# Performance work log

Measured on AMD Instinct MI355X. Metric: run time of the kernel, lower is better.

## Reference

```python
import jax, jax.numpy as jnp
import numpy as np

N = 10000   # nodes
E = 160000  # edges (avg degree 16)
C = 128     # channels (multiplicity)
RB = 8      # radial basis size
HID = 64    # radial MLP hidden
AVG_NEIGH = 16.0

# e3nn-style constants: w3j(1,1,0)=delta/sqrt(3); component-normalization path alphas
C_000 = float(np.sqrt(0.5))                 # 0e x 0e -> 0e (two paths into 0e)
C_110 = float(np.sqrt(0.5) / np.sqrt(3.0))  # 1o x 1o -> 0e
C_011 = float(np.sqrt(1.5) / np.sqrt(3.0))  # 0e x 1o -> 1o (sqrt(dim=3 / 2 paths) * w3j)
C_101 = float(np.sqrt(1.5) / np.sqrt(3.0))  # 1o x 0e -> 1o


def setup_inputs() -> dict:
    key = jax.random.key(0)
    ks = jax.random.split(key, 14)
    rn = lambda k, s: jax.random.normal(k, s, dtype=jnp.float32)
    return {
        "node_attrs": rn(ks[0], (N, 10)),            # unused in forward (kept for fidelity)
        "node_feats": rn(ks[1], (N, 4 * C)),          # 128x0e (128) + 128x1o (384)
        "edge_attrs": rn(ks[2], (E, 4)),              # 1x0e + 1x1o spherical harmonics
        "edge_feats": rn(ks[3], (E, RB)),             # radial basis
        "edge_index": jax.random.randint(ks[4], (2, E), 0, N, dtype=jnp.int32),
        # linear_up (per-irrep channel mixing)
        "W_up_s": rn(ks[5], (C, C)),
        "W_up_v": rn(ks[6], (C, C)),
        # radial MLP [RB,64,64,64,weight_numel=4*C]
        "W_mlp1": rn(ks[7], (RB, HID)),
        "W_mlp2": rn(ks[8], (HID, HID)),
        "W_mlp3": rn(ks[9], (HID, HID)),
        "W_mlp4": rn(ks[10], (HID, 4 * C)),
        # output linear: 256x0e+256x1o -> 128x0e+128x1o
        "W_lin_s": rn(ks[11], (2 * C, C)),
        "W_lin_v": rn(ks[12], (2 * C, C)),
    }


def reference(node_attrs, node_feats, edge_attrs, edge_feats, edge_index,
              W_up_s, W_up_v, W_mlp1, W_mlp2, W_mlp3, W_mlp4, W_lin_s, W_lin_v):
    n = node_feats.shape[0]
    e = edge_feats.shape[0]
    sender, receiver = edge_index[0], edge_index[1]

    # split node feats into scalar (0e) and vector (1o) irreps
    s = node_feats[:, :C]                        # [N, C]
    v = node_feats[:, C:].reshape(n, C, 3)       # [N, C, 3]

    # linear_up: per-irrep channel mixing, e3nn fan-in normalization
    s = s @ (W_up_s / jnp.sqrt(jnp.float32(C)))
    v = jnp.einsum('ncm,cd->ndm', v, W_up_v / jnp.sqrt(jnp.float32(C)))

    # radial MLP -> per-edge tensor-product weights [E, 4, C]
    h = jax.nn.silu(edge_feats @ (W_mlp1 / jnp.sqrt(jnp.float32(RB))))
    h = jax.nn.silu(h @ (W_mlp2 / jnp.sqrt(jnp.float32(HID))))
    h = jax.nn.silu(h @ (W_mlp3 / jnp.sqrt(jnp.float32(HID))))
    tpw = (h @ (W_mlp4 / jnp.sqrt(jnp.float32(HID)))).reshape(e, 4, C)

    # gather sender features
    se = s[sender]                               # [E, C]
    ve = v[sender]                               # [E, C, 3]
    y0 = edge_attrs[:, :1]                       # [E, 1]
    y1 = edge_attrs[:, 1:4]                      # [E, 3]

    # uvu tensor product paths with per-edge weights
    m0a = C_000 * tpw[:, 0] * se * y0                                   # 0e x 0e -> 0e, [E,C]
    m0b = C_110 * tpw[:, 3] * jnp.einsum('ecm,em->ec', ve, y1)          # 1o x 1o -> 0e, [E,C]
    m1a = C_011 * tpw[:, 1][:, :, None] * se[:, :, None] * y1[:, None]  # 0e x 1o -> 1o, [E,C,3]
    m1b = C_101 * tpw[:, 2][:, :, None] * ve * y0[:, :, None]           # 1o x 0e -> 1o, [E,C,3]

    mji_s = jnp.concatenate([m0a, m0b], axis=1)   # [E, 2C]  (256x0e)
    mji_v = jnp.concatenate([m1a, m1b], axis=1)   # [E, 2C, 3] (256x1o)

    # scatter-sum over receiver
    msg_s = jax.ops.segment_sum(mji_s, receiver, num_segments=n)
    msg_v = jax.ops.segment_sum(mji_v, receiver, num_segments=n)

    # output linear (per-irrep) and /avg_num_neighbors
    out_s = msg_s @ (W_lin_s / jnp.sqrt(jnp.float32(2 * C)))
    out_v = jnp.einsum('ncm,cd->ndm', msg_v, W_lin_v / jnp.sqrt(jnp.float32(2 * C)))
    out = jnp.concatenate([out_s, out_v.reshape(n, 3 * C)], axis=1) / AVG_NEIGH
    return out
```

## Files before the change

### kernel.cpp

```cpp
#include <hip/hip_runtime.h>


#define N_NODES 10000
#define N_EDGES 160000

#define SVP_OFF    0u
#define MSG_OFF    2560000u
#define WP_OFF     7680000u
#define ROW_OFF    7749632u
#define SNDS_OFF   7919636u
#define EAS_OFF    8079636u
#define EFS_OFF    8719636u
#define TPW_OFF    9999636u

typedef __attribute__((ext_vector_type(8))) short bf16x8;
typedef __attribute__((ext_vector_type(4))) float f32x4;

__device__ __forceinline__ float silu(float x) {
    return x / (1.0f + __expf(-x));
}
__device__ __forceinline__ short f2bf(float x) {
    unsigned u = __float_as_uint(x);
    unsigned r = (u + 0x7FFFu + ((u >> 16) & 1u)) >> 16;
    return (short)r;
}
__device__ __forceinline__ unsigned cvtpk(float lo, float hi) {
    unsigned r;
    asm("v_cvt_pk_bf16_f32 %0, %1, %2" : "=v"(r) : "v"(lo), "v"(hi));
    return r;
}
__device__ __forceinline__ float bf2f(unsigned h) {
    return __uint_as_float(h << 16);
}

constexpr float INV_SQRT_C  = 0.08838834764831845f;
constexpr float INV_SQRT_RB = 0.35355339059327373f;
constexpr float INV_SQRT_H  = 0.125f;
constexpr float OUT_SCALE   = 0.0625f * 0.0625f;
constexpr float C000 = 0.7071067811865476f;
constexpr float C110 = 0.4082482904638631f;
constexpr float C011 = 0.7071067811865476f;
constexpr float C101 = 0.7071067811865476f;

__global__ void k_pack(const float* __restrict__ W2, const float* __restrict__ W3,
                       const float* __restrict__ W4,
                       const float* __restrict__ Wls, const float* __restrict__ Wlv,
                       const float* __restrict__ Wus, const float* __restrict__ Wuv,
                       short* __restrict__ Wp) {
    int idx = blockIdx.x * 256 + threadIdx.x;
    if (idx < 4096) {
        int i2 = idx;
        int e = i2 & 7, l = (i2 >> 3) & 63, kt = (i2 >> 9) & 1, nt = i2 >> 10;
        int k = kt * 32 + (l >> 4) * 8 + e;
        int col = nt * 16 + (l & 15);
        Wp[idx] = f2bf(W2[k * 64 + col] * INV_SQRT_H);
    } else if (idx < 8192) {
        int i2 = idx - 4096;
        int e = i2 & 7, l = (i2 >> 3) & 63, kt = (i2 >> 9) & 1, nt = i2 >> 10;
        int k = kt * 32 + (l >> 4) * 8 + e;
        int col = nt * 16 + (l & 15);
        Wp[idx] = f2bf(W3[k * 64 + col] * INV_SQRT_H);
    } else if (idx < 40960) {
        int i2 = idx - 8192;
        int e = i2 & 7, l = (i2 >> 3) & 63, kt = (i2 >> 9) & 1, nt = i2 >> 10;
        int k = kt * 32 + (l >> 4) * 8 + e;
        int o = nt * 16 + (l & 15);
        int c = o >> 2, a = o & 3;
        Wp[idx] = f2bf(W4[k * 512 + a * 128 + c] * INV_SQRT_H);
    } else if (idx < 73728) {
        int i2 = idx - 40960;
        int e = i2 & 7, l = (i2 >> 3) & 63, kt = (i2 >> 9) & 7, nt = (i2 >> 12) & 7;
        int k = kt * 32 + (l >> 4) * 8 + e;
        int d = nt * 16 + (l & 15);
        Wp[idx] = f2bf(Wls[k * 128 + d] * OUT_SCALE);
    } else if (idx < 106496) {
        int i2 = idx - 73728;
        int e = i2 & 7, l = (i2 >> 3) & 63, kt = (i2 >> 9) & 7, nt = (i2 >> 12) & 7;
        int k = kt * 32 + (l >> 4) * 8 + e;
        int d = nt * 16 + (l & 15);
        Wp[idx] = f2bf(Wlv[k * 128 + d] * OUT_SCALE);
    } else if (idx < 122880) {
        int i2 = idx - 106496;
        int e = i2 & 7, l = (i2 >> 3) & 63, kt = (i2 >> 9) & 3, nt = (i2 >> 11) & 7;
        int k = kt * 32 + (l >> 4) * 8 + e;
        int d = nt * 16 + (l & 15);
        Wp[idx] = f2bf(Wus[k * 128 + d] * INV_SQRT_C);
    } else if (idx < 139264) {
        int i2 = idx - 122880;
        int e = i2 & 7, l = (i2 >> 3) & 63, kt = (i2 >> 9) & 3, nt = (i2 >> 11) & 7;
        int k = kt * 32 + (l >> 4) * 8 + e;
        int d = nt * 16 + (l & 15);
        Wp[idx] = f2bf(Wuv[k * 128 + d] * INV_SQRT_C);
    }
}

__global__ __launch_bounds__(512) void k_node_up(
    const float* __restrict__ nf,
    const short* __restrict__ Wusp,
    const short* __restrict__ Wuvp,
    uint2*       __restrict__ svp) {
    __shared__ short stage[16 * 128 * 4];

    const int tid = threadIdx.x;
    const int l   = tid & 63;
    const int w   = tid >> 6;
    const int sec = w & 3;
    const int nth = w >> 2;
    const int r16 = l & 15;
    const int g4  = l >> 4;
    const int n0  = blockIdx.x * 16;
    const float* nfrow = nf + (size_t)(n0 + r16) * 512;

    bf16x8 a[4];
    if (sec == 0) {
        #pragma unroll
        for (int kt = 0; kt < 4; ++kt) {
            const float* p = nfrow + kt * 32 + g4 * 8;
            float4 x0 = *(const float4*)p;
            float4 x1 = *(const float4*)(p + 4);
            bf16x8 t;
            t[0] = f2bf(x0.x); t[1] = f2bf(x0.y); t[2] = f2bf(x0.z); t[3] = f2bf(x0.w);
            t[4] = f2bf(x1.x); t[5] = f2bf(x1.y); t[6] = f2bf(x1.z); t[7] = f2bf(x1.w);
            a[kt] = t;
        }
    } else {
        const int m = sec - 1;
        #pragma unroll
        for (int kt = 0; kt < 4; ++kt) {
            const float* p = nfrow + 128 + 3 * (kt * 32 + g4 * 8) + m;
            bf16x8 t;
            #pragma unroll
            for (int e = 0; e < 8; ++e) t[e] = f2bf(p[3 * e]);
            a[kt] = t;
        }
    }
    const short* Wp = (sec == 0) ? Wusp : Wuvp;
    #pragma unroll
    for (int ni = 0; ni < 4; ++ni) {
        const int nt = nth * 4 + ni;
        f32x4 c = {0.f, 0.f, 0.f, 0.f};
        #pragma unroll
        for (int kt = 0; kt < 4; ++kt) {
            bf16x8 b = *(const bf16x8*)(Wp + ((nt * 4 + kt) * 64 + l) * 8);
            c = __builtin_amdgcn_mfma_f32_16x16x32_bf16(a[kt], b, c, 0, 0, 0);
        }
        const int d = nt * 16 + r16;
        #pragma unroll
        for (int r = 0; r < 4; ++r) {
            const int nl = g4 * 4 + r;
            stage[(nl * 128 + d) * 4 + sec] = f2bf(c[r]);
        }
    }
    __syncthreads();
    const uint2* st = (const uint2*)stage;
    uint2* outp = svp + (size_t)n0 * 128;
    #pragma unroll
    for (int j = 0; j < 4; ++j) {
        const int idx = tid + 512 * j;
        outp[idx] = st[idx];
    }
}

__global__ void k_hist(const int* __restrict__ ei, int* __restrict__ cnt) {
    int e = blockIdx.x * 256 + threadIdx.x;
    if (e < N_EDGES) atomicAdd(&cnt[ei[N_EDGES + e]], 1);
}

__global__ void k_scan(const int* __restrict__ cnt, int* __restrict__ row,
                       int* __restrict__ cursor) {
    __shared__ int part[256];
    const int t = threadIdx.x;
    const int base = t * 40;
    int s = 0;
    for (int i = 0; i < 40; ++i) {
        int idx = base + i;
        s += (idx < N_NODES) ? cnt[idx] : 0;
    }
    part[t] = s;
    __syncthreads();
    for (int off = 1; off < 256; off <<= 1) {
        int v = (t >= off) ? part[t - off] : 0;
        __syncthreads();
        part[t] += v;
        __syncthreads();
    }
    int run = part[t] - s;
    for (int i = 0; i < 40; ++i) {
        int idx = base + i;
        if (idx < N_NODES) {
            row[idx] = run;
            cursor[idx] = run;
            run += cnt[idx];
        }
    }
    if (t == 255) row[N_NODES] = part[255];
}

__global__ void k_scatter(const int* __restrict__ ei, int* __restrict__ cursor,
                          const float* __restrict__ edge_attrs,
                          const float* __restrict__ edge_feats,
                          int* __restrict__ snds,
                          float4* __restrict__ eas, float4* __restrict__ efs) {
    int e = blockIdx.x * 256 + threadIdx.x;
    if (e < N_EDGES) {
        int snd = ei[e];
        int r = ei[N_EDGES + e];
        int pos = atomicAdd(&cursor[r], 1);
        snds[pos] = snd;
        eas[pos] = ((const float4*)edge_attrs)[e];
        efs[(size_t)pos * 2 + 0] = ((const float4*)edge_feats)[(size_t)e * 2 + 0];
        efs[(size_t)pos * 2 + 1] = ((const float4*)edge_feats)[(size_t)e * 2 + 1];
    }
}

__global__ __launch_bounds__(256) void k_edge_mfma(
    const float4* __restrict__ efs,
    const float* __restrict__ W1,
    const short* __restrict__ W2p,
    const short* __restrict__ W3p,
    const short* __restrict__ W4p,
    int ne,
    unsigned short* __restrict__ tpw16) {
    __shared__ __align__(16) short h0[64][72];
    __shared__ __align__(16) short h1[64][72];
    __shared__ __align__(16) uint2 stg[4][16][17];

    const int tid = threadIdx.x;
    const int l   = tid & 63;
    const int w   = tid >> 6;
    const int r16 = l & 15;
    const int g4  = l >> 4;
    const int base = blockIdx.x * 64;
    const int erow = w * 16 + r16;

    {
        const int pos = base + erow;
        const size_t p = (size_t)((pos < ne) ? pos : 0);
        float4 f0 = efs[p * 2 + 0];
        float4 f1 = efs[p * 2 + 1];
        float ef[8] = {f0.x, f0.y, f0.z, f0.w, f1.x, f1.y, f1.z, f1.w};
        const int j0 = g4 * 16;
        float acc[16];
        #pragma unroll
        for (int jj = 0; jj < 16; ++jj) acc[jj] = 0.f;
        #pragma unroll
        for (int k = 0; k < 8; ++k) {
            const float* wr = W1 + k * 64 + j0;
            float4 w0 = *(const float4*)(wr + 0);
            float4 w1 = *(const float4*)(wr + 4);
            float4 w2 = *(const float4*)(wr + 8);
            float4 w3 = *(const float4*)(wr + 12);
            const float hk = ef[k];
            acc[0]  = fmaf(hk, w0.x, acc[0]);  acc[1]  = fmaf(hk, w0.y, acc[1]);
            acc[2]  = fmaf(hk, w0.z, acc[2]);  acc[3]  = fmaf(hk, w0.w, acc[3]);
            acc[4]  = fmaf(hk, w1.x, acc[4]);  acc[5]  = fmaf(hk, w1.y, acc[5]);
            acc[6]  = fmaf(hk, w1.z, acc[6]);  acc[7]  = fmaf(hk, w1.w, acc[7]);
            acc[8]  = fmaf(hk, w2.x, acc[8]);  acc[9]  = fmaf(hk, w2.y, acc[9]);
            acc[10] = fmaf(hk, w2.z, acc[10]); acc[11] = fmaf(hk, w2.w, acc[11]);
            acc[12] = fmaf(hk, w3.x, acc[12]); acc[13] = fmaf(hk, w3.y, acc[13]);
            acc[14] = fmaf(hk, w3.z, acc[14]); acc[15] = fmaf(hk, w3.w, acc[15]);
        }
        unsigned pk[8];
        #pragma unroll
        for (int q = 0; q < 8; ++q)
            pk[q] = cvtpk(silu(acc[2*q] * INV_SQRT_RB),
                          silu(acc[2*q + 1] * INV_SQRT_RB));
        uint4 A; A.x = pk[0]; A.y = pk[1]; A.z = pk[2]; A.w = pk[3];
        uint4 B; B.x = pk[4]; B.y = pk[5]; B.z = pk[6]; B.w = pk[7];
        *(uint4*)&h0[erow][j0]     = A;
        *(uint4*)&h0[erow][j0 + 8] = B;
    }

    {
        bf16x8 a0 = *(const bf16x8*)&h0[erow][g4 * 8];
        bf16x8 a1 = *(const bf16x8*)&h0[erow][32 + g4 * 8];
        #pragma unroll
        for (int nt = 0; nt < 4; ++nt) {
            bf16x8 b0 = *(const bf16x8*)(W2p + ((nt * 2 + 0) * 64 + l) * 8);
            bf16x8 b1 = *(const bf16x8*)(W2p + ((nt * 2 + 1) * 64 + l) * 8);
            f32x4 c = {0.f, 0.f, 0.f, 0.f};
            c = __builtin_amdgcn_mfma_f32_16x16x32_bf16(a0, b0, c, 0, 0, 0);
            c = __builtin_amdgcn_mfma_f32_16x16x32_bf16(a1, b1, c, 0, 0, 0);
            unsigned u01 = cvtpk(silu(c[0]), silu(c[1]));
            unsigned u23 = cvtpk(silu(c[2]), silu(c[3]));
            h1[w * 16 + g4 * 4 + 0][nt * 16 + r16] = (short)(u01 & 0xffffu);
            h1[w * 16 + g4 * 4 + 1][nt * 16 + r16] = (short)(u01 >> 16);
            h1[w * 16 + g4 * 4 + 2][nt * 16 + r16] = (short)(u23 & 0xffffu);
            h1[w * 16 + g4 * 4 + 3][nt * 16 + r16] = (short)(u23 >> 16);
        }
    }

    {
        bf16x8 a0 = *(const bf16x8*)&h1[erow][g4 * 8];
        bf16x8 a1 = *(const bf16x8*)&h1[erow][32 + g4 * 8];
        #pragma unroll
        for (int nt = 0; nt < 4; ++nt) {
            bf16x8 b0 = *(const bf16x8*)(W3p + ((nt * 2 + 0) * 64 + l) * 8);
            bf16x8 b1 = *(const bf16x8*)(W3p + ((nt * 2 + 1) * 64 + l) * 8);
            f32x4 c = {0.f, 0.f, 0.f, 0.f};
            c = __builtin_amdgcn_mfma_f32_16x16x32_bf16(a0, b0, c, 0, 0, 0);
            c = __builtin_amdgcn_mfma_f32_16x16x32_bf16(a1, b1, c, 0, 0, 0);
            unsigned u01 = cvtpk(silu(c[0]), silu(c[1]));
            unsigned u23 = cvtpk(silu(c[2]), silu(c[3]));
            h0[w * 16 + g4 * 4 + 0][nt * 16 + r16] = (short)(u01 & 0xffffu);
            h0[w * 16 + g4 * 4 + 1][nt * 16 + r16] = (short)(u01 >> 16);
            h0[w * 16 + g4 * 4 + 2][nt * 16 + r16] = (short)(u23 & 0xffffu);
            h0[w * 16 + g4 * 4 + 3][nt * 16 + r16] = (short)(u23 >> 16);
        }
    }

    {
        bf16x8 ha0 = *(const bf16x8*)&h0[erow][g4 * 8];
        bf16x8 ha1 = *(const bf16x8*)&h0[erow][32 + g4 * 8];
        const int ebase = base + w * 16;
        const int er = (l >> 3) & 7;
        const int ck = l & 7;
        const bool v0 = (ebase + er) < ne;
        const bool v1 = (ebase + er + 8) < ne;
        unsigned short* twb0 = tpw16 + (size_t)(ebase + er) * 512 + ck * 8;
        unsigned short* twb1 = tpw16 + (size_t)(ebase + er + 8) * 512 + ck * 8;
        uint2 (*sw)[17] = stg[w];

        #pragma unroll 2
        for (int grp = 0; grp < 8; ++grp) {
            #pragma unroll
            for (int h = 0; h < 4; ++h) {
                const int nt = grp * 4 + h;
                bf16x8 w0 = *(const bf16x8*)(W4p + ((nt * 2 + 0) * 64 + l) * 8);
                bf16x8 w1 = *(const bf16x8*)(W4p + ((nt * 2 + 1) * 64 + l) * 8);
                f32x4 c = {0.f, 0.f, 0.f, 0.f};
                c = __builtin_amdgcn_mfma_f32_16x16x32_bf16(w0, ha0, c, 0, 0, 0);
                c = __builtin_amdgcn_mfma_f32_16x16x32_bf16(w1, ha1, c, 0, 0, 0);
                uint2 u;
                u.x = cvtpk(c[0], c[1]);
                u.y = cvtpk(c[2], c[3]);
                sw[r16][h * 4 + g4] = u;
            }
            uint2 a0 = sw[er][ck * 2];
            uint2 a1 = sw[er][ck * 2 + 1];
            uint2 b0 = sw[er + 8][ck * 2];
            uint2 b1 = sw[er + 8][ck * 2 + 1];
            if (v0) {
                uint4 v; v.x = a0.x; v.y = a0.y; v.z = a1.x; v.w = a1.y;
                *(uint4*)(twb0 + grp * 64) = v;
            }
            if (v1) {
                uint4 v; v.x = b0.x; v.y = b0.y; v.z = b1.x; v.w = b1.y;
                *(uint4*)(twb1 + grp * 64) = v;
            }
        }
    }
}

__global__ __launch_bounds__(128) void k_gather(
    const int*    __restrict__ row,
    const int*    __restrict__ snds,
    const float4* __restrict__ eas,
    const unsigned short* __restrict__ tpw16,
    const uint2*  __restrict__ svp,
    unsigned short* __restrict__ msg16) {
    const int nidx = blockIdx.x;
    const int c = threadIdx.x;
    const int beg = row[nidx];
    const int end = row[nidx + 1];

    float a0 = 0.f, a1 = 0.f, a2 = 0.f, a3 = 0.f,
          a4 = 0.f, a5 = 0.f, a6 = 0.f, a7 = 0.f;

    #pragma unroll 4
    for (int i = beg; i < end; ++i) {
        const int snd = snds[i];
        const float4 ea = eas[i];
        const float y0 = ea.x, y10 = ea.y, y11 = ea.z, y12 = ea.w;

        const uint2 u  = *(const uint2*)(tpw16 + (size_t)i * 512 + c * 4);
        const uint2 sv = svp[(size_t)snd * 128 + c];
        const float t0 = bf2f(u.x & 0xffffu);
        const float t1 = bf2f(u.x >> 16);
        const float t2 = bf2f(u.y & 0xffffu);
        const float t3 = bf2f(u.y >> 16);
        const float se  = bf2f(sv.x & 0xffffu);
        const float ve0 = bf2f(sv.x >> 16);
        const float ve1 = bf2f(sv.y & 0xffffu);
        const float ve2 = bf2f(sv.y >> 16);

        a0 = fmaf(C000 * t0 * y0, se, a0);
        const float dvy = ve0 * y10 + ve1 * y11 + ve2 * y12;
        a1 = fmaf(C110 * t3, dvy, a1);
        const float c011t = C011 * t1 * se;
        a2 = fmaf(c011t, y10, a2);
        a3 = fmaf(c011t, y11, a3);
        a4 = fmaf(c011t, y12, a4);
        const float c101t = C101 * t2 * y0;
        a5 = fmaf(c101t, ve0, a5);
        a6 = fmaf(c101t, ve1, a6);
        a7 = fmaf(c101t, ve2, a7);
    }

    unsigned short* m = msg16 + (size_t)nidx * 1024;
    m[c]       = (unsigned short)f2bf(a0);
    m[128 + c] = (unsigned short)f2bf(a1);
    m[256 + c] = (unsigned short)f2bf(a2);
    m[512 + c] = (unsigned short)f2bf(a3);
    m[768 + c] = (unsigned short)f2bf(a4);
    m[384 + c] = (unsigned short)f2bf(a5);
    m[640 + c] = (unsigned short)f2bf(a6);
    m[896 + c] = (unsigned short)f2bf(a7);
}

__global__ __launch_bounds__(512) void k_node_out(
    const unsigned short* __restrict__ msg16,
    const short* __restrict__ Wlsp,
    const short* __restrict__ Wlvp,
    float*       __restrict__ out) {
    const int tid = threadIdx.x;
    const int l   = tid & 63;
    const int w   = tid >> 6;
    const int sec = w & 3;
    const int nth = w >> 2;
    const int r16 = l & 15;
    const int g4  = l >> 4;
    const int n0  = blockIdx.x * 16;
    const unsigned short* mrow = msg16 + (size_t)(n0 + r16) * 1024 + sec * 256;

    bf16x8 a[8];
    #pragma unroll
    for (int kt = 0; kt < 8; ++kt)
        a[kt] = *(const bf16x8*)(mrow + kt * 32 + g4 * 8);

    const short* Wp = (sec == 0) ? Wlsp : Wlvp;
    #pragma unroll
    for (int ni = 0; ni < 4; ++ni) {
        const int nt = nth * 4 + ni;
        f32x4 c = {0.f, 0.f, 0.f, 0.f};
        #pragma unroll
        for (int kt = 0; kt < 8; ++kt) {
            bf16x8 b = *(const bf16x8*)(Wp + ((nt * 8 + kt) * 64 + l) * 8);
            c = __builtin_amdgcn_mfma_f32_16x16x32_bf16(a[kt], b, c, 0, 0, 0);
        }
        const int d = nt * 16 + r16;
        #pragma unroll
        for (int r = 0; r < 4; ++r) {
            const size_t n = n0 + g4 * 4 + r;
            if (sec == 0) out[n * 512 + d] = c[r];
            else          out[n * 512 + 128 + 3 * d + (sec - 1)] = c[r];
        }
    }
}

extern "C" void kernel_launch(void* const* d_in, const int* in_sizes, int n_in,
                              void* d_out, int out_size, void* d_ws, size_t ws_size,
                              hipStream_t stream) {
    const float* node_feats = (const float*)d_in[1];
    const float* edge_attrs = (const float*)d_in[2];
    const float* edge_feats = (const float*)d_in[3];
    const int*   edge_index = (const int*)d_in[4];
    const float* W_up_s = (const float*)d_in[5];
    const float* W_up_v = (const float*)d_in[6];
    const float* W_mlp1 = (const float*)d_in[7];
    const float* W_mlp2 = (const float*)d_in[8];
    const float* W_mlp3 = (const float*)d_in[9];
    const float* W_mlp4 = (const float*)d_in[10];
    const float* W_lin_s = (const float*)d_in[11];
    const float* W_lin_v = (const float*)d_in[12];

    float* ws     = (float*)d_ws;
    uint2* svp    = (uint2*)(ws + SVP_OFF);
    unsigned short* msg16 = (unsigned short*)(ws + MSG_OFF);
    short* Wp     = (short*)(ws + WP_OFF);
    short* W2p    = Wp;
    short* W3p    = Wp + 4096;
    short* W4p    = Wp + 8192;
    short* Wlsp   = Wp + 40960;
    short* Wlvp   = Wp + 73728;
    short* Wusp   = Wp + 106496;
    short* Wuvp   = Wp + 122880;
    int*   row    = (int*)(ws + ROW_OFF);
    int*   snds   = (int*)(ws + SNDS_OFF);
    float4* eas   = (float4*)(ws + EAS_OFF);
    float4* efs   = (float4*)(ws + EFS_OFF);
    unsigned short* tpw16 = (unsigned short*)(ws + TPW_OFF);
    int*   cnt    = (int*)msg16;
    int*   cursor = cnt + N_NODES;
    float* out_f  = (float*)d_out;

    (void)hipMemsetAsync(cnt, 0, 2 * N_NODES * sizeof(int), stream);
    k_pack<<<544, 256, 0, stream>>>(W_mlp2, W_mlp3, W_mlp4, W_lin_s, W_lin_v,
                                    W_up_s, W_up_v, Wp);
    k_node_up<<<625, 512, 0, stream>>>(node_feats, Wusp, Wuvp, svp);
    k_hist<<<N_EDGES / 256, 256, 0, stream>>>(edge_index, cnt);
    k_scan<<<1, 256, 0, stream>>>(cnt, row, cursor);
    k_scatter<<<N_EDGES / 256, 256, 0, stream>>>(edge_index, cursor, edge_attrs,
                                                 edge_feats, snds, eas, efs);
    k_edge_mfma<<<(N_EDGES + 63) / 64, 256, 0, stream>>>(
        efs, W_mlp1, W2p, W3p, W4p, N_EDGES, tpw16);
    k_gather<<<N_NODES, 128, 0, stream>>>(row, snds, eas, tpw16, svp, msg16);
    k_node_out<<<625, 512, 0, stream>>>(msg16, Wlsp, Wlvp, out_f);
}
```

Before: 206.5 us.

## Merge independent launches and compute edge MLP in original edge order

```diff
diff --git a/kernel.cpp b/kernel.cpp
--- a/kernel.cpp
+++ b/kernel.cpp
@@ -8,10 +8,15 @@
 #define MSG_OFF    2560000u
 #define WP_OFF     7680000u
 #define ROW_OFF    7749632u
+#define ELIST_OFF  7759636u
 #define SNDS_OFF   7919636u
 #define EAS_OFF    8079636u
-#define EFS_OFF    8719636u
-#define TPW_OFF    9999636u
+#define TPW_OFF    8719636u
+
+#define K1_PACK    272
+#define K1_HIST    313
+#define K3_SCAT    625
+#define K3_EDGE    2500
 
 typedef __attribute__((ext_vector_type(8))) short bf16x8;
 typedef __attribute__((ext_vector_type(4))) float f32x4;
@@ -42,73 +47,120 @@
 constexpr float C011 = 0.7071067811865476f;
 constexpr float C101 = 0.7071067811865476f;
 
-__global__ void k_pack(const float* __restrict__ W2, const float* __restrict__ W3,
-                       const float* __restrict__ W4,
-                       const float* __restrict__ Wls, const float* __restrict__ Wlv,
-                       const float* __restrict__ Wus, const float* __restrict__ Wuv,
-                       short* __restrict__ Wp) {
-    int idx = blockIdx.x * 256 + threadIdx.x;
-    if (idx < 4096) {
-        int i2 = idx;
-        int e = i2 & 7, l = (i2 >> 3) & 63, kt = (i2 >> 9) & 1, nt = i2 >> 10;
-        int k = kt * 32 + (l >> 4) * 8 + e;
-        int col = nt * 16 + (l & 15);
-        Wp[idx] = f2bf(W2[k * 64 + col] * INV_SQRT_H);
-    } else if (idx < 8192) {
-        int i2 = idx - 4096;
-        int e = i2 & 7, l = (i2 >> 3) & 63, kt = (i2 >> 9) & 1, nt = i2 >> 10;
-        int k = kt * 32 + (l >> 4) * 8 + e;
-        int col = nt * 16 + (l & 15);
-        Wp[idx] = f2bf(W3[k * 64 + col] * INV_SQRT_H);
-    } else if (idx < 40960) {
-        int i2 = idx - 8192;
-        int e = i2 & 7, l = (i2 >> 3) & 63, kt = (i2 >> 9) & 1, nt = i2 >> 10;
-        int k = kt * 32 + (l >> 4) * 8 + e;
-        int o = nt * 16 + (l & 15);
-        int c = o >> 2, a = o & 3;
-        Wp[idx] = f2bf(W4[k * 512 + a * 128 + c] * INV_SQRT_H);
-    } else if (idx < 73728) {
-        int i2 = idx - 40960;
-        int e = i2 & 7, l = (i2 >> 3) & 63, kt = (i2 >> 9) & 7, nt = (i2 >> 12) & 7;
-        int k = kt * 32 + (l >> 4) * 8 + e;
-        int d = nt * 16 + (l & 15);
-        Wp[idx] = f2bf(Wls[k * 128 + d] * OUT_SCALE);
-    } else if (idx < 106496) {
-        int i2 = idx - 73728;
-        int e = i2 & 7, l = (i2 >> 3) & 63, kt = (i2 >> 9) & 7, nt = (i2 >> 12) & 7;
-        int k = kt * 32 + (l >> 4) * 8 + e;
-        int d = nt * 16 + (l & 15);
-        Wp[idx] = f2bf(Wlv[k * 128 + d] * OUT_SCALE);
-    } else if (idx < 122880) {
-        int i2 = idx - 106496;
-        int e = i2 & 7, l = (i2 >> 3) & 63, kt = (i2 >> 9) & 3, nt = (i2 >> 11) & 7;
-        int k = kt * 32 + (l >> 4) * 8 + e;
-        int d = nt * 16 + (l & 15);
-        Wp[idx] = f2bf(Wus[k * 128 + d] * INV_SQRT_C);
-    } else if (idx < 139264) {
-        int i2 = idx - 122880;
-        int e = i2 & 7, l = (i2 >> 3) & 63, kt = (i2 >> 9) & 3, nt = (i2 >> 11) & 7;
-        int k = kt * 32 + (l >> 4) * 8 + e;
-        int d = nt * 16 + (l & 15);
-        Wp[idx] = f2bf(Wuv[k * 128 + d] * INV_SQRT_C);
-    }
-}
-
-__global__ __launch_bounds__(512) void k_node_up(
+__global__ __launch_bounds__(512) void k1_pack_hist(
+    const float* __restrict__ W2, const float* __restrict__ W3,
+    const float* __restrict__ W4,
+    const float* __restrict__ Wls, const float* __restrict__ Wlv,
+    const float* __restrict__ Wus, const float* __restrict__ Wuv,
+    short* __restrict__ Wp,
+    const int* __restrict__ ei, int* __restrict__ cnt) {
+    const int bid = blockIdx.x;
+    const int tid = threadIdx.x;
+
+    if (bid < K1_PACK) {
+        int idx = bid * 512 + tid;
+        if (idx < 4096) {
+            int i2 = idx;
+            int e = i2 & 7, l = (i2 >> 3) & 63, kt = (i2 >> 9) & 1, nt = i2 >> 10;
+            int k = kt * 32 + (l >> 4) * 8 + e;
+            int col = nt * 16 + (l & 15);
+            Wp[idx] = f2bf(W2[k * 64 + col] * INV_SQRT_H);
+        } else if (idx < 8192) {
+            int i2 = idx - 4096;
+            int e = i2 & 7, l = (i2 >> 3) & 63, kt = (i2 >> 9) & 1, nt = i2 >> 10;
+            int k = kt * 32 + (l >> 4) * 8 + e;
+            int col = nt * 16 + (l & 15);
+            Wp[idx] = f2bf(W3[k * 64 + col] * INV_SQRT_H);
+        } else if (idx < 40960) {
+            int i2 = idx - 8192;
+            int e = i2 & 7, l = (i2 >> 3) & 63, kt = (i2 >> 9) & 1, nt = i2 >> 10;
+            int k = kt * 32 + (l >> 4) * 8 + e;
+            int o = nt * 16 + (l & 15);
+            int c = o >> 2, a = o & 3;
+            Wp[idx] = f2bf(W4[k * 512 + a * 128 + c] * INV_SQRT_H);
+        } else if (idx < 73728) {
+            int i2 = idx - 40960;
+            int e = i2 & 7, l = (i2 >> 3) & 63, kt = (i2 >> 9) & 7, nt = (i2 >> 12) & 7;
+            int k = kt * 32 + (l >> 4) * 8 + e;
+            int d = nt * 16 + (l & 15);
+            Wp[idx] = f2bf(Wls[k * 128 + d] * OUT_SCALE);
+        } else if (idx < 106496) {
+            int i2 = idx - 73728;
+            int e = i2 & 7, l = (i2 >> 3) & 63, kt = (i2 >> 9) & 7, nt = (i2 >> 12) & 7;
+            int k = kt * 32 + (l >> 4) * 8 + e;
+            int d = nt * 16 + (l & 15);
+            Wp[idx] = f2bf(Wlv[k * 128 + d] * OUT_SCALE);
+        } else if (idx < 122880) {
+            int i2 = idx - 106496;
+            int e = i2 & 7, l = (i2 >> 3) & 63, kt = (i2 >> 9) & 3, nt = (i2 >> 11) & 7;
+            int k = kt * 32 + (l >> 4) * 8 + e;
+            int d = nt * 16 + (l & 15);
+            Wp[idx] = f2bf(Wus[k * 128 + d] * INV_SQRT_C);
+        } else if (idx < 139264) {
+            int i2 = idx - 122880;
+            int e = i2 & 7, l = (i2 >> 3) & 63, kt = (i2 >> 9) & 3, nt = (i2 >> 11) & 7;
+            int k = kt * 32 + (l >> 4) * 8 + e;
+            int d = nt * 16 + (l & 15);
+            Wp[idx] = f2bf(Wuv[k * 128 + d] * INV_SQRT_C);
+        }
+        return;
+    }
+    int e = (bid - K1_PACK) * 512 + tid;
+    if (e < N_EDGES) atomicAdd(&cnt[ei[N_EDGES + e]], 1);
+}
+
+__global__ __launch_bounds__(512) void k2_scan_nodeup(
+    const int*   __restrict__ cnt,
+    int*         __restrict__ row,
+    int*         __restrict__ cursor,
     const float* __restrict__ nf,
-    const short* __restrict__ Wusp,
-    const short* __restrict__ Wuvp,
+    const short* __restrict__ Wp,
     uint2*       __restrict__ svp) {
-    __shared__ short stage[16 * 128 * 4];
-
+    __shared__ __align__(8) short stage[16 * 128 * 4];
+    const int bid = blockIdx.x;
     const int tid = threadIdx.x;
+
+    if (bid == 0) {
+        int* part = (int*)stage;
+        const int t = tid;
+        const int base = t * 20;
+        int s = 0;
+        #pragma unroll
+        for (int i = 0; i < 20; ++i) {
+            int idx = base + i;
+            s += (idx < N_NODES) ? cnt[idx] : 0;
+        }
+        part[t] = s;
+        __syncthreads();
+        for (int off = 1; off < 512; off <<= 1) {
+            int v = (t >= off) ? part[t - off] : 0;
+            __syncthreads();
+            part[t] += v;
+            __syncthreads();
+        }
+        int run = part[t] - s;
+        #pragma unroll
+        for (int i = 0; i < 20; ++i) {
+            int idx = base + i;
+            if (idx < N_NODES) {
+                row[idx] = run;
+                cursor[idx] = run;
+                run += cnt[idx];
+            }
+        }
+        if (t == 511) row[N_NODES] = part[511];
+        return;
+    }
+
+    const short* Wusp = Wp + 106496;
+    const short* Wuvp = Wp + 122880;
     const int l   = tid & 63;
     const int w   = tid >> 6;
     const int sec = w & 3;
     const int nth = w >> 2;
     const int r16 = l & 15;
     const int g4  = l >> 4;
-    const int n0  = blockIdx.x * 16;
+    const int n0  = (bid - 1) * 16;
     const float* nfrow = nf + (size_t)(n0 + r16) * 512;
 
     bf16x8 a[4];
@@ -134,14 +186,14 @@
             a[kt] = t;
         }
     }
-    const short* Wp = (sec == 0) ? Wusp : Wuvp;
+    const short* Wq = (sec == 0) ? Wusp : Wuvp;
     #pragma unroll
     for (int ni = 0; ni < 4; ++ni) {
         const int nt = nth * 4 + ni;
         f32x4 c = {0.f, 0.f, 0.f, 0.f};
         #pragma unroll
         for (int kt = 0; kt < 4; ++kt) {
-            bf16x8 b = *(const bf16x8*)(Wp + ((nt * 4 + kt) * 64 + l) * 8);
+            bf16x8 b = *(const bf16x8*)(Wq + ((nt * 4 + kt) * 64 + l) * 8);
             c = __builtin_amdgcn_mfma_f32_16x16x32_bf16(a[kt], b, c, 0, 0, 0);
         }
         const int d = nt * 16 + r16;
@@ -161,83 +213,51 @@
     }
 }
 
-__global__ void k_hist(const int* __restrict__ ei, int* __restrict__ cnt) {
-    int e = blockIdx.x * 256 + threadIdx.x;
-    if (e < N_EDGES) atomicAdd(&cnt[ei[N_EDGES + e]], 1);
-}
-
-__global__ void k_scan(const int* __restrict__ cnt, int* __restrict__ row,
-                       int* __restrict__ cursor) {
-    __shared__ int part[256];
-    const int t = threadIdx.x;
-    const int base = t * 40;
-    int s = 0;
-    for (int i = 0; i < 40; ++i) {
-        int idx = base + i;
-        s += (idx < N_NODES) ? cnt[idx] : 0;
-    }
-    part[t] = s;
-    __syncthreads();
-    for (int off = 1; off < 256; off <<= 1) {
-        int v = (t >= off) ? part[t - off] : 0;
-        __syncthreads();
-        part[t] += v;
-        __syncthreads();
-    }
-    int run = part[t] - s;
-    for (int i = 0; i < 40; ++i) {
-        int idx = base + i;
-        if (idx < N_NODES) {
-            row[idx] = run;
-            cursor[idx] = run;
-            run += cnt[idx];
-        }
-    }
-    if (t == 255) row[N_NODES] = part[255];
-}
-
-__global__ void k_scatter(const int* __restrict__ ei, int* __restrict__ cursor,
-                          const float* __restrict__ edge_attrs,
-                          const float* __restrict__ edge_feats,
-                          int* __restrict__ snds,
-                          float4* __restrict__ eas, float4* __restrict__ efs) {
-    int e = blockIdx.x * 256 + threadIdx.x;
-    if (e < N_EDGES) {
-        int snd = ei[e];
-        int r = ei[N_EDGES + e];
-        int pos = atomicAdd(&cursor[r], 1);
-        snds[pos] = snd;
-        eas[pos] = ((const float4*)edge_attrs)[e];
-        efs[(size_t)pos * 2 + 0] = ((const float4*)edge_feats)[(size_t)e * 2 + 0];
-        efs[(size_t)pos * 2 + 1] = ((const float4*)edge_feats)[(size_t)e * 2 + 1];
-    }
-}
-
-__global__ __launch_bounds__(256) void k_edge_mfma(
-    const float4* __restrict__ efs,
+__global__ __launch_bounds__(256) void k3_scat_edge(
+    const int*   __restrict__ ei,
+    int*         __restrict__ cursor,
+    const float* __restrict__ edge_attrs,
+    int*         __restrict__ elist,
+    int*         __restrict__ snds,
+    float4*      __restrict__ eas,
+    const float* __restrict__ edge_feats,
     const float* __restrict__ W1,
-    const short* __restrict__ W2p,
-    const short* __restrict__ W3p,
-    const short* __restrict__ W4p,
-    int ne,
+    const short* __restrict__ Wp,
     unsigned short* __restrict__ tpw16) {
     __shared__ __align__(16) short h0[64][72];
     __shared__ __align__(16) short h1[64][72];
     __shared__ __align__(16) uint2 stg[4][16][17];
 
+    const int bid = blockIdx.x;
     const int tid = threadIdx.x;
+
+    if (bid < K3_SCAT) {
+        int e = bid * 256 + tid;
+        if (e < N_EDGES) {
+            int snd = ei[e];
+            int r = ei[N_EDGES + e];
+            int pos = atomicAdd(&cursor[r], 1);
+            elist[pos] = e;
+            snds[pos] = snd;
+            eas[pos] = ((const float4*)edge_attrs)[e];
+        }
+        return;
+    }
+
+    const short* W2p = Wp;
+    const short* W3p = Wp + 4096;
+    const short* W4p = Wp + 8192;
     const int l   = tid & 63;
     const int w   = tid >> 6;
     const int r16 = l & 15;
     const int g4  = l >> 4;
-    const int base = blockIdx.x * 64;
+    const int base = (bid - K3_SCAT) * 64;
     const int erow = w * 16 + r16;
 
     {
-        const int pos = base + erow;
-        const size_t p = (size_t)((pos < ne) ? pos : 0);
-        float4 f0 = efs[p * 2 + 0];
-        float4 f1 = efs[p * 2 + 1];
+        const size_t p = (size_t)(base + erow);
+        float4 f0 = ((const float4*)edge_feats)[p * 2 + 0];
+        float4 f1 = ((const float4*)edge_feats)[p * 2 + 1];
         float ef[8] = {f0.x, f0.y, f0.z, f0.w, f1.x, f1.y, f1.z, f1.w};
         const int j0 = g4 * 16;
         float acc[16];
@@ -315,8 +335,6 @@
         const int ebase = base + w * 16;
         const int er = (l >> 3) & 7;
         const int ck = l & 7;
-        const bool v0 = (ebase + er) < ne;
-        const bool v1 = (ebase + er + 8) < ne;
         unsigned short* twb0 = tpw16 + (size_t)(ebase + er) * 512 + ck * 8;
         unsigned short* twb1 = tpw16 + (size_t)(ebase + er + 8) * 512 + ck * 8;
         uint2 (*sw)[17] = stg[w];
@@ -340,11 +358,11 @@
             uint2 a1 = sw[er][ck * 2 + 1];
             uint2 b0 = sw[er + 8][ck * 2];
             uint2 b1 = sw[er + 8][ck * 2 + 1];
-            if (v0) {
+            {
                 uint4 v; v.x = a0.x; v.y = a0.y; v.z = a1.x; v.w = a1.y;
                 *(uint4*)(twb0 + grp * 64) = v;
             }
-            if (v1) {
+            {
                 uint4 v; v.x = b0.x; v.y = b0.y; v.z = b1.x; v.w = b1.y;
                 *(uint4*)(twb1 + grp * 64) = v;
             }
@@ -354,6 +372,7 @@
 
 __global__ __launch_bounds__(128) void k_gather(
     const int*    __restrict__ row,
+    const int*    __restrict__ elist,
     const int*    __restrict__ snds,
     const float4* __restrict__ eas,
     const unsigned short* __restrict__ tpw16,
@@ -369,11 +388,12 @@
 
     #pragma unroll 4
     for (int i = beg; i < end; ++i) {
+        const int e   = elist[i];
         const int snd = snds[i];
         const float4 ea = eas[i];
         const float y0 = ea.x, y10 = ea.y, y11 = ea.z, y12 = ea.w;
 
-        const uint2 u  = *(const uint2*)(tpw16 + (size_t)i * 512 + c * 4);
+        const uint2 u  = *(const uint2*)(tpw16 + (size_t)e * 512 + c * 4);
         const uint2 sv = svp[(size_t)snd * 128 + c];
         const float t0 = bf2f(u.x & 0xffffu);
         const float t1 = bf2f(u.x >> 16);
@@ -428,14 +448,14 @@
     for (int kt = 0; kt < 8; ++kt)
         a[kt] = *(const bf16x8*)(mrow + kt * 32 + g4 * 8);
 
-    const short* Wp = (sec == 0) ? Wlsp : Wlvp;
+    const short* Wq = (sec == 0) ? Wlsp : Wlvp;
     #pragma unroll
     for (int ni = 0; ni < 4; ++ni) {
         const int nt = nth * 4 + ni;
         f32x4 c = {0.f, 0.f, 0.f, 0.f};
         #pragma unroll
         for (int kt = 0; kt < 8; ++kt) {
-            bf16x8 b = *(const bf16x8*)(Wp + ((nt * 8 + kt) * 64 + l) * 8);
+            bf16x8 b = *(const bf16x8*)(Wq + ((nt * 8 + kt) * 64 + l) * 8);
             c = __builtin_amdgcn_mfma_f32_16x16x32_bf16(a[kt], b, c, 0, 0, 0);
         }
         const int d = nt * 16 + r16;
@@ -468,32 +488,26 @@
     uint2* svp    = (uint2*)(ws + SVP_OFF);
     unsigned short* msg16 = (unsigned short*)(ws + MSG_OFF);
     short* Wp     = (short*)(ws + WP_OFF);
-    short* W2p    = Wp;
-    short* W3p    = Wp + 4096;
-    short* W4p    = Wp + 8192;
     short* Wlsp   = Wp + 40960;
     short* Wlvp   = Wp + 73728;
-    short* Wusp   = Wp + 106496;
-    short* Wuvp   = Wp + 122880;
     int*   row    = (int*)(ws + ROW_OFF);
+    int*   elist  = (int*)(ws + ELIST_OFF);
     int*   snds   = (int*)(ws + SNDS_OFF);
     float4* eas   = (float4*)(ws + EAS_OFF);
-    float4* efs   = (float4*)(ws + EFS_OFF);
     unsigned short* tpw16 = (unsigned short*)(ws + TPW_OFF);
     int*   cnt    = (int*)msg16;
     int*   cursor = cnt + N_NODES;
     float* out_f  = (float*)d_out;
 
     (void)hipMemsetAsync(cnt, 0, 2 * N_NODES * sizeof(int), stream);
-    k_pack<<<544, 256, 0, stream>>>(W_mlp2, W_mlp3, W_mlp4, W_lin_s, W_lin_v,
-                                    W_up_s, W_up_v, Wp);
-    k_node_up<<<625, 512, 0, stream>>>(node_feats, Wusp, Wuvp, svp);
-    k_hist<<<N_EDGES / 256, 256, 0, stream>>>(edge_index, cnt);
-    k_scan<<<1, 256, 0, stream>>>(cnt, row, cursor);
-    k_scatter<<<N_EDGES / 256, 256, 0, stream>>>(edge_index, cursor, edge_attrs,
-                                                 edge_feats, snds, eas, efs);
-    k_edge_mfma<<<(N_EDGES + 63) / 64, 256, 0, stream>>>(
-        efs, W_mlp1, W2p, W3p, W4p, N_EDGES, tpw16);
-    k_gather<<<N_NODES, 128, 0, stream>>>(row, snds, eas, tpw16, svp, msg16);
+    k1_pack_hist<<<K1_PACK + K1_HIST, 512, 0, stream>>>(
+        W_mlp2, W_mlp3, W_mlp4, W_lin_s, W_lin_v, W_up_s, W_up_v, Wp,
+        edge_index, cnt);
+    k2_scan_nodeup<<<1 + 625, 512, 0, stream>>>(
+        cnt, row, cursor, node_feats, Wp, svp);
+    k3_scat_edge<<<K3_SCAT + K3_EDGE, 256, 0, stream>>>(
+        edge_index, cursor, edge_attrs, elist, snds, eas,
+        edge_feats, W_mlp1, Wp, tpw16);
+    k_gather<<<N_NODES, 128, 0, stream>>>(row, elist, snds, eas, tpw16, svp, msg16);
     k_node_out<<<625, 512, 0, stream>>>(msg16, Wlsp, Wlvp, out_f);
 }
```

Measured after the change: 195.8 us. 5.2% less time.
